# Kernel optimization log

Hardware: AMD Instinct MI355X
Metric: run time of the kernel (lower is better)

The kernel has to match this reference:

```python
import jax, jax.numpy as jnp
import numpy as np

NUM_SLOTS = 64
MEMORY_DIM = 512
EMBED_DIM = 1024
SCALE = MEMORY_DIM ** (-0.5)


def setup_inputs() -> dict:
    key = jax.random.key(0)
    ks = jax.random.split(key, 7)
    B, S, E, Dm = 8, 4096, EMBED_DIM, MEMORY_DIM
    s = 0.02
    return {
        "embeddings": jax.random.normal(ks[0], (B, S, E), dtype=jnp.float32),
        "W_write": jax.random.normal(ks[1], (E, Dm), dtype=jnp.float32) * s,
        "b_write": jnp.zeros((Dm,), dtype=jnp.float32),
        "W_query": jax.random.normal(ks[2], (E, Dm), dtype=jnp.float32) * s,
        "b_query": jnp.zeros((Dm,), dtype=jnp.float32),
        "W_out": jax.random.normal(ks[3], (Dm, E), dtype=jnp.float32) * s,
        "b_out": jnp.zeros((E,), dtype=jnp.float32),
    }


def reference(embeddings, W_write, b_write, W_query, b_query, W_out, b_out):
    B, S, E = embeddings.shape
    M, Dm = NUM_SLOTS, MEMORY_DIM
    # Precompute per-token projections (linear, so identical to per-step).
    write_vals = jnp.einsum('bse,ed->bsd', embeddings, W_write) + b_write  # [B,S,Dm]
    queries = jnp.einsum('bse,ed->bsd', embeddings, W_query) + b_query      # [B,S,Dm]
    addrs = jnp.arange(S) % M  # hash(position) = position % M

    def step(carry, xs):
        memory, written = carry            # [B,M,Dm], [B,M] bool
        q, wv, addr = xs                   # [B,Dm], [B,Dm], scalar int
        # read BEFORE write (current token not yet in memory)
        sim = jnp.einsum('bd,bmd->bm', q, memory) * SCALE
        sim = jnp.where(written, sim, -jnp.inf)
        attn = jax.nn.softmax(sim, axis=-1)
        attn = jnp.nan_to_num(attn)        # all-unwritten -> zeros
        retrieved = jnp.einsum('bm,bmd->bd', attn, memory)
        memory = memory.at[:, addr, :].set(wv)
        written = written.at[:, addr].set(True)
        return (memory, written), retrieved

    mem0 = jnp.zeros((B, M, Dm), dtype=embeddings.dtype)
    wr0 = jnp.zeros((B, M), dtype=bool)
    xs = (queries.transpose(1, 0, 2), write_vals.transpose(1, 0, 2), addrs)
    _, retrieved = jax.lax.scan(step, (mem0, wr0), xs)  # [S,B,Dm]
    retrieved = retrieved.transpose(1, 0, 2)            # [B,S,Dm]
    # read_out is linear per-step -> apply once over the whole sequence
    return jnp.einsum('bsd,de->bse', retrieved, W_out) + b_out
```

## Files before the change

kernel.cpp:

```cpp
#include <hip/hip_runtime.h>
#include <hip/hip_bf16.h>
#include <math.h>


#define BATCH   8
#define S_LEN   4096
#define EMB     1024
#define DM      512
#define MROWS   (BATCH * S_LEN)
#define SCALE_F 0.04419417382415922f

typedef __attribute__((ext_vector_type(4))) float f32x4;
typedef __attribute__((ext_vector_type(8))) short short8;

__device__ __forceinline__ unsigned short f2bf(float f) {
    __hip_bfloat16 h = __float2bfloat16(f);
    return *reinterpret_cast<unsigned short*>(&h);
}

__global__ __launch_bounds__(256) void prep(
    const float4* __restrict__ emb4, ushort4* __restrict__ embb4,
    const float* __restrict__ W_wr, const float* __restrict__ W_qr,
    const float* __restrict__ W_out,
    const float* __restrict__ b_wr, const float* __restrict__ b_qr,
    __hip_bfloat16* __restrict__ wcat, __hip_bfloat16* __restrict__ wout,
    float* __restrict__ bcat)
{
    const int bx = blockIdx.x;
    if (bx < 32768) {
        int id = bx * 256 + threadIdx.x;
        float4 v = emb4[id];
        ushort4 o;
        o.x = f2bf(v.x); o.y = f2bf(v.y); o.z = f2bf(v.z); o.w = f2bf(v.w);
        embb4[id] = o;
    } else if (bx < 32768 + 2048) {
        int id = (bx - 32768) * 256 + threadIdx.x;
        int n = id >> 10, k = id & 1023;
        wcat[id] = __float2bfloat16(W_wr[k * 512 + n]);
    } else if (bx < 32768 + 4096) {
        int id = (bx - 32768 - 2048) * 256 + threadIdx.x;
        int n = id >> 10, k = id & 1023;
        wcat[(size_t)DM * EMB + id] = __float2bfloat16(W_qr[k * 512 + n]);
    } else if (bx < 32768 + 6144) {
        int id = (bx - 32768 - 4096) * 256 + threadIdx.x;
        int n = id >> 9, k = id & 511;
        wout[id] = __float2bfloat16(W_out[k * 1024 + n]);
    } else {
        int i = threadIdx.x;
#pragma unroll
        for (int r = 0; r < 4; ++r, i += 256)
            bcat[i] = (i < 512) ? b_wr[i] : b_qr[i - 512];
    }
}

template<bool BF16OUT, bool TRANSLO>
__global__ __launch_bounds__(512, 2) void gemm256(
    const __hip_bfloat16* __restrict__ A, int lda,
    const __hip_bfloat16* __restrict__ Bt, int ldb,
    const float* __restrict__ bias,
    void* __restrict__ Cv, int ldc,
    __hip_bfloat16* __restrict__ wvtp,
    int K, int nbx)
{
    __shared__ __align__(16) char smem[131072];

    const int nwg = gridDim.x;
    const int bid = blockIdx.x;
    const int cpx = nwg >> 3;
    const int swz = (bid & 7) * cpx + (bid >> 3);
    const int bm0 = (swz / nbx) << 8;
    const int bn0 = (swz % nbx) << 8;

    const int tid  = threadIdx.x;
    const int lane = tid & 63;
    const int w    = tid >> 6;
    const int wm   = w >> 2, wn = w & 3;
    const int l15  = lane & 15, lhi = lane >> 4;
    const int nt   = K >> 6;

    const int r64 = tid >> 3;
    const int cg8 = ((tid & 7) ^ (r64 & 7)) << 3;

    auto stage_tile = [&](int buf, int kt) {
#pragma unroll
        for (int h = 0; h < 4; ++h) {
            const int isB = h >> 1, hh = h & 1;
            const __hip_bfloat16* G = isB ? Bt : A;
            const int ldg = isB ? ldb : lda;
            const int rb  = (isB ? bn0 : bm0) + hh * 128;
#pragma unroll
            for (int i = 0; i < 2; ++i) {
                const __hip_bfloat16* g =
                    G + (size_t)(rb + i * 64 + r64) * ldg + kt + cg8;
                char* l = smem + buf * 65536 + isB * 32768 + hh * 16384
                          + i * 8192 + w * 1024;
                __builtin_amdgcn_global_load_lds(
                    (const __attribute__((address_space(1))) unsigned int*)g,
                    (__attribute__((address_space(3))) unsigned int*)l, 16, 0, 0);
            }
        }
    };

    f32x4 acc[8][4] = {};

    stage_tile(0, 0);
    __syncthreads();

    for (int t = 0; t < nt; ++t) {
        const int cur = t & 1;
        const bool pf = (t + 1 < nt);
        if (pf) stage_tile(cur ^ 1, (t + 1) << 6);

        const char* sA = smem + cur * 65536;
        const char* sB = sA + 32768;

        short8 bfv[2][2][2];
#pragma unroll
        for (int nh = 0; nh < 2; ++nh)
#pragma unroll
            for (int ni = 0; ni < 2; ++ni) {
                const int r = wn * 64 + nh * 32 + ni * 16 + l15;
#pragma unroll
                for (int kk = 0; kk < 2; ++kk) {
                    const int pc = (kk * 4 + lhi) ^ (r & 7);
                    bfv[nh][ni][kk] = *(const short8*)(sB + r * 128 + (pc << 4));
                }
            }

#pragma unroll
        for (int mh = 0; mh < 2; ++mh) {
            short8 af[4][2];
#pragma unroll
            for (int mi = 0; mi < 4; ++mi) {
                const int r = wm * 128 + mh * 64 + mi * 16 + l15;
#pragma unroll
                for (int kk = 0; kk < 2; ++kk) {
                    const int pc = (kk * 4 + lhi) ^ (r & 7);
                    af[mi][kk] = *(const short8*)(sA + r * 128 + (pc << 4));
                }
            }
#pragma unroll
            for (int nh = 0; nh < 2; ++nh)
#pragma unroll
                for (int mi = 0; mi < 4; ++mi)
#pragma unroll
                    for (int ni = 0; ni < 2; ++ni)
#pragma unroll
                        for (int kk = 0; kk < 2; ++kk)
                            acc[mh * 4 + mi][nh * 2 + ni] =
                                __builtin_amdgcn_mfma_f32_16x16x32_bf16(
                                    af[mi][kk], bfv[nh][ni][kk],
                                    acc[mh * 4 + mi][nh * 2 + ni], 0, 0, 0);
        }

        if (pf) __syncthreads();
    }

    float bv[4];
#pragma unroll
    for (int N = 0; N < 4; ++N)
        bv[N] = bias[bn0 + wn * 64 + (N >> 1) * 32 + (N & 1) * 16 + l15];

#pragma unroll
    for (int M = 0; M < 8; ++M) {
        const int row = bm0 + wm * 128 + (M >> 2) * 64 + (M & 3) * 16 + lhi * 4;
#pragma unroll
        for (int N = 0; N < 4; ++N) {
            const int col = bn0 + wn * 64 + (N >> 1) * 32 + (N & 1) * 16 + l15;
            float v[4];
#pragma unroll
            for (int reg = 0; reg < 4; ++reg)
                v[reg] = acc[M][N][reg] + bv[N];

#pragma unroll
            for (int reg = 0; reg < 4; ++reg) {
                if (BF16OUT)
                    ((__hip_bfloat16*)Cv)[(size_t)(row + reg) * ldc + col] =
                        __float2bfloat16(v[reg]);
                else
                    ((float*)Cv)[(size_t)(row + reg) * ldc + col] = v[reg];
            }
            if (TRANSLO && col < 512) {
                union { unsigned short s[4]; uint2 u; } tv;
#pragma unroll
                for (int reg = 0; reg < 4; ++reg) tv.s[reg] = f2bf(v[reg]);
                *(uint2*)((unsigned short*)wvtp
                          + (((size_t)((row >> 12) * 512 + col)) << 12)
                          + (row & 4095)) = tv.u;
            }
        }
    }
}

__global__ __launch_bounds__(256) void attn_mfma(
    const __hip_bfloat16* __restrict__ WVQ,
    const __hip_bfloat16* __restrict__ WVT,
    __hip_bfloat16* __restrict__ R)
{
    __shared__ __align__(16) unsigned short p_lds[64][136];

    const int blk0 = blockIdx.x;
    const int blk  = (blk0 & 7) * 64 + (blk0 >> 3);
    const int b   = blk >> 6;
    const int t0  = (blk & 63) << 6;
    const int jmin = (t0 == 0) ? 64 : 0;
    const size_t bbase = (size_t)b << 12;
    const int tid  = threadIdx.x;
    const int lane = tid & 63;
    const int w    = tid >> 6;
    const int l15  = lane & 15;
    const int lhi  = lane >> 4;

    f32x4 acc[8] = {};
    const __hip_bfloat16* q0 =
        WVQ + ((bbase + t0 + w * 16 + l15) << 10) + 512 + lhi * 8;

    const __hip_bfloat16* brow[8];
#pragma unroll
    for (int nt = 0; nt < 8; ++nt) {
        int aj = t0 - 64 + nt * 16 + l15;
        if (aj < 0) aj = 0;
        brow[nt] = WVQ + ((bbase + aj) << 10) + lhi * 8;
    }

#pragma unroll 2
    for (int kt = 0; kt < 16; ++kt) {
        short8 qa = *(const short8*)(q0 + kt * 32);
#pragma unroll
        for (int nt = 0; nt < 8; ++nt) {
            short8 bv = *(const short8*)(brow[nt] + kt * 32);
            acc[nt] = __builtin_amdgcn_mfma_f32_16x16x32_bf16(qa, bv, acc[nt], 0, 0, 0);
        }
    }

    float m4[4] = { -1e30f, -1e30f, -1e30f, -1e30f };
#pragma unroll
    for (int nt = 0; nt < 8; ++nt)
#pragma unroll
        for (int reg = 0; reg < 4; ++reg) {
            int i = w * 16 + lhi * 4 + reg;
            int j = nt * 16 + l15;
            bool valid = (j >= i) && (j <= i + 63) && (j >= jmin);
            float s = valid ? acc[nt][reg] * SCALE_F : -1e30f;
            acc[nt][reg] = s;
            m4[reg] = fmaxf(m4[reg], s);
        }
#pragma unroll
    for (int off = 8; off >= 1; off >>= 1)
#pragma unroll
        for (int reg = 0; reg < 4; ++reg)
            m4[reg] = fmaxf(m4[reg], __shfl_xor(m4[reg], off, 64));

    float sum4[4] = {};
#pragma unroll
    for (int nt = 0; nt < 8; ++nt)
#pragma unroll
        for (int reg = 0; reg < 4; ++reg) {
            float s = acc[nt][reg];
            float p = (s > -1e29f) ? __expf(s - m4[reg]) : 0.f;
            acc[nt][reg] = p;
            sum4[reg] += p;
        }
#pragma unroll
    for (int off = 8; off >= 1; off >>= 1)
#pragma unroll
        for (int reg = 0; reg < 4; ++reg)
            sum4[reg] += __shfl_xor(sum4[reg], off, 64);

    float rs4[4];
#pragma unroll
    for (int reg = 0; reg < 4; ++reg)
        rs4[reg] = (sum4[reg] > 0.f) ? 1.f / sum4[reg] : 0.f;

#pragma unroll
    for (int nt = 0; nt < 8; ++nt)
#pragma unroll
        for (int reg = 0; reg < 4; ++reg)
            p_lds[w * 16 + lhi * 4 + reg][nt * 16 + l15] =
                f2bf(acc[nt][reg] * rs4[reg]);

    __syncthreads();

    short8 pa[4];
#pragma unroll
    for (int kt = 0; kt < 4; ++kt)
        pa[kt] = *(const short8*)&p_lds[w * 16 + l15][kt * 32 + lhi * 8];

    int tclamp[4];
#pragma unroll
    for (int kt = 0; kt < 4; ++kt) {
        int ti = t0 - 64 + kt * 32 + lhi * 8;
        tclamp[kt] = ti < 0 ? 0 : ti;
    }

    const size_t vbase = (size_t)b * 512;
#pragma unroll 2
    for (int nt = 0; nt < 32; ++nt) {
        int d = nt * 16 + l15;
        f32x4 a = {};
#pragma unroll
        for (int kt = 0; kt < 4; ++kt) {
            short8 bv = *(const short8*)(WVT + ((vbase + d) << 12) + tclamp[kt]);
            a = __builtin_amdgcn_mfma_f32_16x16x32_bf16(pa[kt], bv, a, 0, 0, 0);
        }
        size_t rb = (bbase + t0 + w * 16 + lhi * 4) << 9;
#pragma unroll
        for (int reg = 0; reg < 4; ++reg)
            R[rb + ((size_t)reg << 9) + d] = __float2bfloat16(a[reg]);
    }
}

extern "C" void kernel_launch(void* const* d_in, const int* in_sizes, int n_in,
                              void* d_out, int out_size, void* d_ws, size_t ws_size,
                              hipStream_t stream)
{
    const float* emb   = (const float*)d_in[0];
    const float* W_wr  = (const float*)d_in[1];
    const float* b_wr  = (const float*)d_in[2];
    const float* W_qr  = (const float*)d_in[3];
    const float* b_qr  = (const float*)d_in[4];
    const float* W_out = (const float*)d_in[5];
    const float* b_out = (const float*)d_in[6];
    float* out = (float*)d_out;

    char* ws = (char*)d_ws;
    __hip_bfloat16* embb = (__hip_bfloat16*)(ws);
    __hip_bfloat16* rbuf = (__hip_bfloat16*)(ws);
    __hip_bfloat16* wvq  = (__hip_bfloat16*)(ws + (((size_t)64) << 20));
    __hip_bfloat16* wvt  = (__hip_bfloat16*)(ws + (((size_t)128) << 20));
    __hip_bfloat16* wcat = (__hip_bfloat16*)(ws + (((size_t)160) << 20));
    __hip_bfloat16* wout = (__hip_bfloat16*)(ws + (((size_t)162) << 20));
    float*          bcat = (float*)        (ws + (((size_t)163) << 20));

    prep<<<dim3(38913), dim3(256), 0, stream>>>(
        (const float4*)emb, (ushort4*)embb,
        W_wr, W_qr, W_out, b_wr, b_qr, wcat, wout, bcat);

    gemm256<true, true><<<dim3(512), dim3(512), 0, stream>>>(
        embb, EMB, wcat, EMB, bcat, (void*)wvq, 1024, wvt, EMB, 4);

    attn_mfma<<<dim3(MROWS / 64), dim3(256), 0, stream>>>(wvq, wvt, rbuf);

    gemm256<false, false><<<dim3(512), dim3(512), 0, stream>>>(
        rbuf, DM, wout, DM, b_out, (void*)out, EMB, nullptr, DM, 4);
}
```

Measured before the change: 238.3 us.

## Interleave GEMM prefetch with MFMA quadrants using fine-grained waitcnt and setprio

Restructures the bf16 GEMM main loop into four MFMA quadrants, issuing the next tile's global-to-LDS loads in pieces between quadrants. A full __syncthreads is replaced by partial vmcnt waits plus raw s_barrier, and s_setprio raises wave priority around MFMA bursts. The goal is to overlap memory traffic with matrix math and cut barrier stalls. The hand-counted vmcnt values and barrier placement must match the load ordering exactly, or the loop can race on LDS buffers.

```diff
diff --git a/kernel.cpp b/kernel.cpp
--- a/kernel.cpp
+++ b/kernel.cpp
@@ -81,79 +81,129 @@
     const int r64 = tid >> 3;
     const int cg8 = ((tid & 7) ^ (r64 & 7)) << 3;
 
-    auto stage_tile = [&](int buf, int kt) {
-#pragma unroll
-        for (int h = 0; h < 4; ++h) {
-            const int isB = h >> 1, hh = h & 1;
-            const __hip_bfloat16* G = isB ? Bt : A;
-            const int ldg = isB ? ldb : lda;
-            const int rb  = (isB ? bn0 : bm0) + hh * 128;
-#pragma unroll
-            for (int i = 0; i < 2; ++i) {
-                const __hip_bfloat16* g =
-                    G + (size_t)(rb + i * 64 + r64) * ldg + kt + cg8;
-                char* l = smem + buf * 65536 + isB * 32768 + hh * 16384
-                          + i * 8192 + w * 1024;
-                __builtin_amdgcn_global_load_lds(
-                    (const __attribute__((address_space(1))) unsigned int*)g,
-                    (__attribute__((address_space(3))) unsigned int*)l, 16, 0, 0);
-            }
-        }
+    auto stageA = [&](int buf, int kt, int r) {
+        const __hip_bfloat16* g =
+            A + (size_t)(bm0 + r * 64 + r64) * lda + kt + cg8;
+        char* l = smem + buf * 65536 + r * 8192 + w * 1024;
+        __builtin_amdgcn_global_load_lds(
+            (const __attribute__((address_space(1))) unsigned int*)g,
+            (__attribute__((address_space(3))) unsigned int*)l, 16, 0, 0);
     };
+    auto stageB = [&](int buf, int kt, int r) {
+        const __hip_bfloat16* g =
+            Bt + (size_t)(bn0 + r * 64 + r64) * ldb + kt + cg8;
+        char* l = smem + buf * 65536 + 32768 + r * 8192 + w * 1024;
+        __builtin_amdgcn_global_load_lds(
+            (const __attribute__((address_space(1))) unsigned int*)g,
+            (__attribute__((address_space(3))) unsigned int*)l, 16, 0, 0);
+    };
 
     f32x4 acc[8][4] = {};
 
-    stage_tile(0, 0);
-    __syncthreads();
+    stageB(0, 0, 0); stageB(0, 0, 1); stageB(0, 0, 2); stageB(0, 0, 3);
+    stageA(0, 0, 0); stageA(0, 0, 2); stageA(0, 0, 1); stageA(0, 0, 3);
+    asm volatile("s_waitcnt vmcnt(2)" ::: "memory");
+    __builtin_amdgcn_s_barrier();
 
     for (int t = 0; t < nt; ++t) {
         const int cur = t & 1;
         const bool pf = (t + 1 < nt);
-        if (pf) stage_tile(cur ^ 1, (t + 1) << 6);
-
+        const int kt1 = (t + 1) << 6;
         const char* sA = smem + cur * 65536;
         const char* sB = sA + 32768;
 
-        short8 bfv[2][2][2];
-#pragma unroll
-        for (int nh = 0; nh < 2; ++nh)
-#pragma unroll
-            for (int ni = 0; ni < 2; ++ni) {
-                const int r = wn * 64 + nh * 32 + ni * 16 + l15;
-#pragma unroll
-                for (int kk = 0; kk < 2; ++kk) {
-                    const int pc = (kk * 4 + lhi) ^ (r & 7);
-                    bfv[nh][ni][kk] = *(const short8*)(sB + r * 128 + (pc << 4));
-                }
-            }
-
-#pragma unroll
-        for (int mh = 0; mh < 2; ++mh) {
-            short8 af[4][2];
-#pragma unroll
-            for (int mi = 0; mi < 4; ++mi) {
-                const int r = wm * 128 + mh * 64 + mi * 16 + l15;
-#pragma unroll
-                for (int kk = 0; kk < 2; ++kk) {
-                    const int pc = (kk * 4 + lhi) ^ (r & 7);
-                    af[mi][kk] = *(const short8*)(sA + r * 128 + (pc << 4));
-                }
-            }
-#pragma unroll
-            for (int nh = 0; nh < 2; ++nh)
-#pragma unroll
-                for (int mi = 0; mi < 4; ++mi)
-#pragma unroll
-                    for (int ni = 0; ni < 2; ++ni)
-#pragma unroll
-                        for (int kk = 0; kk < 2; ++kk)
-                            acc[mh * 4 + mi][nh * 2 + ni] =
-                                __builtin_amdgcn_mfma_f32_16x16x32_bf16(
-                                    af[mi][kk], bfv[nh][ni][kk],
-                                    acc[mh * 4 + mi][nh * 2 + ni], 0, 0, 0);
-        }
-
-        if (pf) __syncthreads();
+        short8 af[4][2], b0[2][2], b1[2][2];
+
+        if (pf) { stageB(cur ^ 1, kt1, 0); stageB(cur ^ 1, kt1, 1); }
+#pragma unroll
+        for (int ni = 0; ni < 2; ++ni) {
+            const int r = wn * 64 + ni * 16 + l15;
+#pragma unroll
+            for (int kk = 0; kk < 2; ++kk) {
+                const int pc = (kk * 4 + lhi) ^ (r & 7);
+                b0[ni][kk] = *(const short8*)(sB + r * 128 + (pc << 4));
+            }
+        }
+#pragma unroll
+        for (int mi = 0; mi < 4; ++mi) {
+            const int r = wm * 128 + mi * 16 + l15;
+#pragma unroll
+            for (int kk = 0; kk < 2; ++kk) {
+                const int pc = (kk * 4 + lhi) ^ (r & 7);
+                af[mi][kk] = *(const short8*)(sA + r * 128 + (pc << 4));
+            }
+        }
+        __builtin_amdgcn_s_setprio(1);
+#pragma unroll
+        for (int mi = 0; mi < 4; ++mi)
+#pragma unroll
+            for (int ni = 0; ni < 2; ++ni)
+#pragma unroll
+                for (int kk = 0; kk < 2; ++kk)
+                    acc[mi][ni] = __builtin_amdgcn_mfma_f32_16x16x32_bf16(
+                        af[mi][kk], b0[ni][kk], acc[mi][ni], 0, 0, 0);
+        __builtin_amdgcn_s_setprio(0);
+
+        if (pf) { stageB(cur ^ 1, kt1, 2); stageB(cur ^ 1, kt1, 3); }
+#pragma unroll
+        for (int ni = 0; ni < 2; ++ni) {
+            const int r = wn * 64 + 32 + ni * 16 + l15;
+#pragma unroll
+            for (int kk = 0; kk < 2; ++kk) {
+                const int pc = (kk * 4 + lhi) ^ (r & 7);
+                b1[ni][kk] = *(const short8*)(sB + r * 128 + (pc << 4));
+            }
+        }
+        __builtin_amdgcn_s_setprio(1);
+#pragma unroll
+        for (int mi = 0; mi < 4; ++mi)
+#pragma unroll
+            for (int ni = 0; ni < 2; ++ni)
+#pragma unroll
+                for (int kk = 0; kk < 2; ++kk)
+                    acc[mi][2 + ni] = __builtin_amdgcn_mfma_f32_16x16x32_bf16(
+                        af[mi][kk], b1[ni][kk], acc[mi][2 + ni], 0, 0, 0);
+        __builtin_amdgcn_s_setprio(0);
+
+        if (pf) { asm volatile("s_waitcnt vmcnt(4)" ::: "memory"); }
+        else    { asm volatile("s_waitcnt vmcnt(0)" ::: "memory"); }
+        __builtin_amdgcn_s_barrier();
+
+        if (pf) { stageA(cur ^ 1, kt1, 0); stageA(cur ^ 1, kt1, 2); }
+#pragma unroll
+        for (int mi = 0; mi < 4; ++mi) {
+            const int r = wm * 128 + 64 + mi * 16 + l15;
+#pragma unroll
+            for (int kk = 0; kk < 2; ++kk) {
+                const int pc = (kk * 4 + lhi) ^ (r & 7);
+                af[mi][kk] = *(const short8*)(sA + r * 128 + (pc << 4));
+            }
+        }
+        __builtin_amdgcn_s_setprio(1);
+#pragma unroll
+        for (int mi = 0; mi < 4; ++mi)
+#pragma unroll
+            for (int ni = 0; ni < 2; ++ni)
+#pragma unroll
+                for (int kk = 0; kk < 2; ++kk)
+                    acc[4 + mi][ni] = __builtin_amdgcn_mfma_f32_16x16x32_bf16(
+                        af[mi][kk], b0[ni][kk], acc[4 + mi][ni], 0, 0, 0);
+        __builtin_amdgcn_s_setprio(0);
+
+        if (pf) { stageA(cur ^ 1, kt1, 1); stageA(cur ^ 1, kt1, 3); }
+        __builtin_amdgcn_s_setprio(1);
+#pragma unroll
+        for (int mi = 0; mi < 4; ++mi)
+#pragma unroll
+            for (int ni = 0; ni < 2; ++ni)
+#pragma unroll
+                for (int kk = 0; kk < 2; ++kk)
+                    acc[4 + mi][2 + ni] = __builtin_amdgcn_mfma_f32_16x16x32_bf16(
+                        af[mi][kk], b1[ni][kk], acc[4 + mi][2 + ni], 0, 0, 0);
+        __builtin_amdgcn_s_setprio(0);
+
+        asm volatile("s_waitcnt vmcnt(2)" ::: "memory");
+        __builtin_amdgcn_s_barrier();
     }
 
     float bv[4];
```

Measured after the change: 240.4 us. No clear change (+0.9%).
